# Performance work log

Measured on AMD Instinct MI355X. Metric: run time of the kernel, lower is better.

Reference implementation:

```python
import jax, jax.numpy as jnp
import numpy as np
import math

V, D, H, L, F, S, B = 32000, 1024, 16, 6, 4096, 1024, 2
HD = D // H
EPS = 1e-5


def _pos_encoding(seq_len, d_model):
    pos = np.arange(seq_len, dtype=np.float32)[:, None]
    div = np.exp(np.arange(0, d_model, 2, dtype=np.float32) * (-math.log(10000.0) / d_model))
    pe = np.zeros((seq_len, d_model), dtype=np.float32)
    pe[:, 0::2] = np.sin(pos * div)
    pe[:, 1::2] = np.cos(pos * div)
    return jnp.asarray(pe)


def setup_inputs() -> dict:
    key = jax.random.key(0)
    ks = jax.random.split(key, 24)
    s = 0.02
    emb = jax.random.normal(ks[0], (V, D), jnp.float32) * s
    emb = emb.at[0].set(0.0)  # padding_idx=0
    return {
        "input_ids": jax.random.randint(ks[1], (B, S), 0, V),
        "emb": emb,
        "Wq": jax.random.normal(ks[2], (L, D, D), jnp.float32) * s,
        "bq": jnp.zeros((L, D), jnp.float32),
        "Wk": jax.random.normal(ks[3], (L, D, D), jnp.float32) * s,
        "bk": jnp.zeros((L, D), jnp.float32),
        "Wv": jax.random.normal(ks[4], (L, D, D), jnp.float32) * s,
        "bv": jnp.zeros((L, D), jnp.float32),
        "Wo": jax.random.normal(ks[5], (L, D, D), jnp.float32) * s,
        "bo": jnp.zeros((L, D), jnp.float32),
        "ln1_g": jnp.ones((L, D), jnp.float32),
        "ln1_b": jnp.zeros((L, D), jnp.float32),
        "ln2_g": jnp.ones((L, D), jnp.float32),
        "ln2_b": jnp.zeros((L, D), jnp.float32),
        "W1": jax.random.normal(ks[6], (L, D, F), jnp.float32) * s,
        "b1": jnp.zeros((L, F), jnp.float32),
        "W2": jax.random.normal(ks[7], (L, F, D), jnp.float32) * s,
        "b2": jnp.zeros((L, D), jnp.float32),
        "fn_g": jnp.ones((D,), jnp.float32),
        "fn_b": jnp.zeros((D,), jnp.float32),
        "Wout": jax.random.normal(ks[8], (D, V), jnp.float32) * s,
        "bout": jnp.zeros((V,), jnp.float32),
    }


def _layernorm(x, g, b):
    m = jnp.mean(x, axis=-1, keepdims=True)
    v = jnp.mean(jnp.square(x - m), axis=-1, keepdims=True)
    return (x - m) * jax.lax.rsqrt(v + EPS) * g + b


def reference(input_ids, emb, Wq, bq, Wk, bk, Wv, bv, Wo, bo,
              ln1_g, ln1_b, ln2_g, ln2_b, W1, b1, W2, b2,
              fn_g, fn_b, Wout, bout):
    b, s = input_ids.shape
    x = emb[input_ids] * math.sqrt(D)          # [B,S,D]
    x = x + _pos_encoding(s, D)[None]           # positional encoding (dropout off: eval)
    causal = jnp.tril(jnp.ones((s, s), dtype=bool))  # True where allowed
    for i in range(L):
        h = _layernorm(x, ln1_g[i], ln1_b[i])
        q = (h @ Wq[i] + bq[i]).reshape(b, s, H, HD).transpose(0, 2, 1, 3)
        k = (h @ Wk[i] + bk[i]).reshape(b, s, H, HD).transpose(0, 2, 1, 3)
        v = (h @ Wv[i] + bv[i]).reshape(b, s, H, HD).transpose(0, 2, 1, 3)
        scores = jnp.einsum('bhqd,bhkd->bhqk', q, k) / math.sqrt(HD)
        scores = jnp.where(causal, scores, -jnp.inf)
        attn = jax.nn.softmax(scores, axis=-1)
        ctx = jnp.einsum('bhqk,bhkd->bhqd', attn, v)
        ctx = ctx.transpose(0, 2, 1, 3).reshape(b, s, D)
        x = x + (ctx @ Wo[i] + bo[i])
        h2 = _layernorm(x, ln2_g[i], ln2_b[i])
        ff = jax.nn.gelu(h2 @ W1[i] + b1[i], approximate=False) @ W2[i] + b2[i]
        x = x + ff
    x = _layernorm(x, fn_g, fn_b)
    logits = x @ Wout + bout                   # [B,S,V]
    return logits
```

## Files before the change

### kernel.cpp

```cpp
#include <hip/hip_runtime.h>
#include <math.h>

#define V_   32000
#define D_   1024
#define H_   16
#define HD_  64
#define L_   6
#define F_   4096
#define S_   1024
#define B_   2
#define MTOK (B_*S_)
#define EPSLN 1e-5f

typedef unsigned short ushort_t;
typedef __attribute__((ext_vector_type(8))) short  s16x8;
typedef __attribute__((ext_vector_type(4))) float  f32x4;
typedef __attribute__((ext_vector_type(4))) unsigned short u16x4;

__device__ __forceinline__ float bf2f(unsigned short u) {
    unsigned int x = ((unsigned int)u) << 16;
    return __builtin_bit_cast(float, x);
}
__device__ __forceinline__ unsigned short f2bf(float f) {
    unsigned int x = __builtin_bit_cast(unsigned int, f);
    unsigned int r = (x + 0x7FFFu + ((x >> 16) & 1u)) >> 16;
    return (unsigned short)r;
}
__device__ __forceinline__ float gelu_f(float x) {
    float y = 0.7978845608f * (x + 0.044715f * x * x * x);
    float t = 1.0f - 2.0f / (__expf(2.0f * y) + 1.0f);
    return 0.5f * x * (1.0f + t);
}

__device__ __forceinline__ float blk_sum(float v, float* sb) {
    #pragma unroll
    for (int o = 32; o; o >>= 1) v += __shfl_xor(v, o, 64);
    int w = threadIdx.x >> 6;
    __syncthreads();
    if ((threadIdx.x & 63) == 0) sb[w] = v;
    __syncthreads();
    return sb[0] + sb[1] + sb[2] + sb[3];
}

template<bool GELU, bool OUTBF>
__global__ __launch_bounds__(512, 2)
void gemm256(const ushort_t* __restrict__ A, int lda,
             const ushort_t* __restrict__ BT, int ldb,
             void* __restrict__ Cv, int ldc,
             const float* __restrict__ bias,
             int M, int N, int K)
{
    int nmt = M >> 8;
    int nwg = gridDim.x * gridDim.y;
    int id  = blockIdx.x + gridDim.x * blockIdx.y;
    int swz = ((nwg & 7) == 0) ? ((id & 7) * (nwg >> 3) + (id >> 3)) : id;
    int m0 = (swz % nmt) << 8;
    int n0 = (swz / nmt) << 8;

    __shared__ __align__(16) ushort_t lA[2][256 * 64];
    __shared__ __align__(16) ushort_t lB[2][256 * 64];

    int tid  = threadIdx.x;
    int lane = tid & 63, wave = tid >> 6;
    int lr = lane & 15, lg = lane >> 4;
    int wm = wave >> 2, wn = wave & 3;

    f32x4 acc[8][4] = {};
    int nkt = K >> 6;

    auto stageu = [&](int buf, int kt, int sel) {
        int k0 = kt << 6;
        const ushort_t* src = (sel < 2) ? A : BT;
        int ld    = (sel < 2) ? lda : ldb;
        int rbase = ((sel < 2) ? m0 : n0) + ((sel & 1) << 7);
        ushort_t* dst = ((sel < 2) ? &lA[buf][0] : &lB[buf][0]) + ((sel & 1) << 13);
        #pragma unroll
        for (int r = 0; r < 2; ++r) {
            int e8  = r * 512 + tid;
            int row = e8 >> 3, slot = e8 & 7;
            int ls  = slot ^ (row & 7);
            const ushort_t* g = src + (size_t)(rbase + row) * ld + k0 + ls * 8;
            __builtin_amdgcn_global_load_lds(
                (const __attribute__((address_space(1))) void*)g,
                (__attribute__((address_space(3))) void*)(dst + e8 * 8), 16, 0, 0);
        }
    };
    auto rdA = [&](int buf, int row, int ks) -> s16x8 {
        int sl = (lg + ks * 4) ^ (row & 7);
        return *(const s16x8*)&lA[buf][row * 64 + sl * 8];
    };
    auto rdB = [&](int buf, int row, int ks) -> s16x8 {
        int sl = (lg + ks * 4) ^ (row & 7);
        return *(const s16x8*)&lB[buf][row * 64 + sl * 8];
    };

    stageu(0, 0, 0); stageu(0, 0, 1); stageu(0, 0, 2); stageu(0, 0, 3);
    if (nkt > 1) {
        stageu(1, 1, 2); stageu(1, 1, 3);
        asm volatile("s_waitcnt vmcnt(4)" ::: "memory");
    } else {
        asm volatile("s_waitcnt vmcnt(0)" ::: "memory");
    }
    __builtin_amdgcn_sched_barrier(0);
    __builtin_amdgcn_s_barrier();

    for (int u = 0; u < nkt; ++u) {
        int cur = u & 1, nxt = cur ^ 1;
        s16x8 af0[4][2], af1[4][2], bf0[2][2], bf1[2][2];

        #pragma unroll
        for (int mf = 0; mf < 4; ++mf)
            #pragma unroll
            for (int ks = 0; ks < 2; ++ks)
                af0[mf][ks] = rdA(cur, wm * 128 + mf * 16 + lr, ks);
        #pragma unroll
        for (int nf = 0; nf < 2; ++nf)
            #pragma unroll
            for (int ks = 0; ks < 2; ++ks) {
                bf0[nf][ks] = rdB(cur, wn * 64 + nf * 16 + lr, ks);
                bf1[nf][ks] = rdB(cur, wn * 64 + 32 + nf * 16 + lr, ks);
            }
        if (u + 1 < nkt) { stageu(nxt, u + 1, 0); stageu(nxt, u + 1, 1); }
        __builtin_amdgcn_s_barrier();
        asm volatile("s_waitcnt lgkmcnt(0)" ::: "memory");
        __builtin_amdgcn_sched_barrier(0);
        __builtin_amdgcn_s_setprio(1);
        #pragma unroll
        for (int mf = 0; mf < 4; ++mf)
            #pragma unroll
            for (int ks = 0; ks < 2; ++ks) {
                #pragma unroll
                for (int nf = 0; nf < 2; ++nf) {
                    acc[mf][nf]     = __builtin_amdgcn_mfma_f32_16x16x32_bf16(
                        af0[mf][ks], bf0[nf][ks], acc[mf][nf], 0, 0, 0);
                    acc[mf][2 + nf] = __builtin_amdgcn_mfma_f32_16x16x32_bf16(
                        af0[mf][ks], bf1[nf][ks], acc[mf][2 + nf], 0, 0, 0);
                }
            }
        __builtin_amdgcn_s_setprio(0);
        __builtin_amdgcn_s_barrier();

        #pragma unroll
        for (int mf = 0; mf < 4; ++mf)
            #pragma unroll
            for (int ks = 0; ks < 2; ++ks)
                af1[mf][ks] = rdA(cur, wm * 128 + 64 + mf * 16 + lr, ks);
        if (u + 2 < nkt) { stageu(cur, u + 2, 2); stageu(cur, u + 2, 3); }
        __builtin_amdgcn_s_barrier();
        asm volatile("s_waitcnt lgkmcnt(0)" ::: "memory");
        __builtin_amdgcn_sched_barrier(0);
        __builtin_amdgcn_s_setprio(1);
        #pragma unroll
        for (int mf = 0; mf < 4; ++mf)
            #pragma unroll
            for (int ks = 0; ks < 2; ++ks) {
                #pragma unroll
                for (int nf = 0; nf < 2; ++nf) {
                    acc[4 + mf][nf]     = __builtin_amdgcn_mfma_f32_16x16x32_bf16(
                        af1[mf][ks], bf0[nf][ks], acc[4 + mf][nf], 0, 0, 0);
                    acc[4 + mf][2 + nf] = __builtin_amdgcn_mfma_f32_16x16x32_bf16(
                        af1[mf][ks], bf1[nf][ks], acc[4 + mf][2 + nf], 0, 0, 0);
                }
            }
        __builtin_amdgcn_s_setprio(0);
        if (u + 2 < nkt) asm volatile("s_waitcnt vmcnt(4)" ::: "memory");
        else             asm volatile("s_waitcnt vmcnt(0)" ::: "memory");
        __builtin_amdgcn_sched_barrier(0);
        __builtin_amdgcn_s_barrier();
    }

    float*    Cf = (float*)Cv;
    ushort_t* Cb = (ushort_t*)Cv;
    #pragma unroll
    for (int mf = 0; mf < 8; ++mf) {
        int gm0 = m0 + wm * 128 + mf * 16 + lg * 4;
        #pragma unroll
        for (int nf = 0; nf < 4; ++nf) {
            int gn = n0 + wn * 64 + nf * 16 + lr;
            float bv = bias ? bias[gn] : 0.f;
            #pragma unroll
            for (int j = 0; j < 4; ++j) {
                float v = acc[mf][nf][j] + bv;
                if (GELU) v = gelu_f(v);
                size_t ci = (size_t)(gm0 + j) * ldc + gn;
                if (OUTBF) Cb[ci] = f2bf(v);
                else       Cf[ci] = v;
            }
        }
    }
}

template<int BN, bool GELU, bool RES, bool OUTBF, bool VOUT>
__global__ __launch_bounds__(256)
void gemm_bt(const ushort_t* __restrict__ A, int lda,
             const ushort_t* __restrict__ BT, int ldb,
             void* __restrict__ Cv, int ldc,
             const float* __restrict__ bias,
             const float* __restrict__ res,
             int M, int N, int K, ushort_t* __restrict__ vtp)
{
    const int BK = 64;
    const int NF = BN / 32;
    int nwg = gridDim.x * gridDim.y;
    int id  = blockIdx.x + gridDim.x * blockIdx.y;
    int swz = ((nwg & 7) == 0) ? ((id & 7) * (nwg >> 3) + (id >> 3)) : id;
    int m0 = (swz % gridDim.x) * 128;
    int n0 = (swz / gridDim.x) * BN;

    __shared__ __align__(16) ushort_t lA[2][128 * BK];
    __shared__ __align__(16) ushort_t lB[2][BN * BK];

    int tid  = threadIdx.x;
    int lane = tid & 63;
    int wave = tid >> 6;
    int lr = lane & 15, lg = lane >> 4;
    int wr = wave >> 1, wc = wave & 1;

    f32x4 acc[4][NF] = {};
    int nkt = K / BK;

    auto stage = [&](int buf, int kt) {
        int k0 = kt * BK;
        #pragma unroll
        for (int i = 0; i < 4; ++i) {
            int e8  = i * 256 + tid;
            int row = e8 >> 3, slot = e8 & 7;
            int ls  = slot ^ (row & 7);
            const ushort_t* g = A + (size_t)(m0 + row) * lda + k0 + ls * 8;
            __builtin_amdgcn_global_load_lds(
                (const __attribute__((address_space(1))) void*)g,
                (__attribute__((address_space(3))) void*)&lA[buf][e8 * 8], 16, 0, 0);
        }
        #pragma unroll
        for (int i = 0; i < BN / 32; ++i) {
            int e8  = i * 256 + tid;
            int row = e8 >> 3, slot = e8 & 7;
            int ls  = slot ^ (row & 7);
            const ushort_t* g = BT + (size_t)(n0 + row) * ldb + k0 + ls * 8;
            __builtin_amdgcn_global_load_lds(
                (const __attribute__((address_space(1))) void*)g,
                (__attribute__((address_space(3))) void*)&lB[buf][e8 * 8], 16, 0, 0);
        }
    };

    stage(0, 0);
    __syncthreads();

    int cur = 0;
    for (int kt = 0; kt < nkt; ++kt) {
        if (kt + 1 < nkt) stage(cur ^ 1, kt + 1);
        __builtin_amdgcn_sched_barrier(0);
        s16x8 af[4][2], bfr[NF][2];
        #pragma unroll
        for (int m = 0; m < 4; ++m) {
            int row = wr * 64 + m * 16 + lr;
            #pragma unroll
            for (int ks = 0; ks < 2; ++ks) {
                int sl = (lg + ks * 4) ^ (row & 7);
                af[m][ks] = *(const s16x8*)&lA[cur][row * BK + sl * 8];
            }
        }
        #pragma unroll
        for (int n = 0; n < NF; ++n) {
            int row = wc * (BN / 2) + n * 16 + lr;
            #pragma unroll
            for (int ks = 0; ks < 2; ++ks) {
                int sl = (lg + ks * 4) ^ (row & 7);
                bfr[n][ks] = *(const s16x8*)&lB[cur][row * BK + sl * 8];
            }
        }
        __builtin_amdgcn_s_setprio(1);
        #pragma unroll
        for (int m = 0; m < 4; ++m)
            #pragma unroll
            for (int n = 0; n < NF; ++n)
                #pragma unroll
                for (int ks = 0; ks < 2; ++ks)
                    acc[m][n] = __builtin_amdgcn_mfma_f32_16x16x32_bf16(
                        af[m][ks], bfr[n][ks], acc[m][n], 0, 0, 0);
        __builtin_amdgcn_s_setprio(0);
        __syncthreads();
        cur ^= 1;
    }

    float*    Cf = (float*)Cv;
    ushort_t* Cb = (ushort_t*)Cv;
    #pragma unroll
    for (int m = 0; m < 4; ++m) {
        int gm0 = m0 + wr * 64 + m * 16 + lg * 4;
        #pragma unroll
        for (int n = 0; n < NF; ++n) {
            int gn = n0 + wc * (BN / 2) + n * 16 + lr;
            #pragma unroll
            for (int j = 0; j < 4; ++j) {
                float v = acc[m][n][j];
                if (bias) v += bias[gn];
                size_t ci = (size_t)(gm0 + j) * ldc + gn;
                if (RES)  v += res[ci];
                if (GELU) v = gelu_f(v);
                if (OUTBF) Cb[ci] = f2bf(v);
                else       Cf[ci] = v;
                if (VOUT && gn >= 2048) {
                    int hv = gn - 2048;
                    int mm = gm0 + j;
                    vtp[((size_t)(((mm >> 10) << 4) + (hv >> 6)) * 64
                         + (hv & 63)) * 1024 + (mm & 1023)] = f2bf(v);
                }
            }
        }
    }
}

__global__ __launch_bounds__(256)
void flash_attn(const ushort_t* __restrict__ qkv,
                const ushort_t* __restrict__ vt,
                ushort_t* __restrict__ ctx)
{
    const int QB = 64, KB = 64;
    int z  = blockIdx.y;
    int b  = z >> 4, hh = z & 15;

    __shared__ __align__(16) ushort_t Qs[QB * 64];
    __shared__ __align__(16) ushort_t Ks[2][KB * 64];
    __shared__ __align__(16) ushort_t Vs[2][64 * KB];
    __shared__ float    Ss[QB][68];
    __shared__ __align__(16) ushort_t Ps[QB][72];
    __shared__ float mrow[QB], lrow[QB], arow[QB];

    int tid  = threadIdx.x;
    int lane = tid & 63, wave = tid >> 6;
    int lr = lane & 15, lg = lane >> 4;
    int r = tid >> 2, p = tid & 3;

    auto stageKV = [&](int buf, int kv0) {
        const ushort_t* kbase = qkv + (size_t)(b * S_ + kv0) * 3072 + 1024 + hh * HD_;
        const ushort_t* vbase = vt + (size_t)z * HD_ * S_ + kv0;
        #pragma unroll
        for (int rnd = 0; rnd < 2; ++rnd) {
            int e8 = rnd * 256 + tid;
            int row = e8 >> 3, slot = e8 & 7;
            int ls = slot ^ (row & 7);
            const ushort_t* gk = kbase + (size_t)row * 3072 + ls * 8;
            __builtin_amdgcn_global_load_lds(
                (const __attribute__((address_space(1))) void*)gk,
                (__attribute__((address_space(3))) void*)&Ks[buf][e8 * 8], 16, 0, 0);
            const ushort_t* gv = vbase + (size_t)row * S_ + ls * 8;
            __builtin_amdgcn_global_load_lds(
                (const __attribute__((address_space(1))) void*)gv,
                (__attribute__((address_space(3))) void*)&Vs[buf][e8 * 8], 16, 0, 0);
        }
    };

    #pragma unroll
    for (int half = 0; half < 2; ++half) {
        int qt = half ? (15 - (int)blockIdx.x) : (int)blockIdx.x;
        int q0 = qt * QB;

        if (tid < QB) { mrow[tid] = -1e30f; lrow[tid] = 0.f; }
        const ushort_t* qbase = qkv + (size_t)(b * S_ + q0) * 3072 + hh * HD_;
        #pragma unroll
        for (int rnd = 0; rnd < 2; ++rnd) {
            int e8   = rnd * 256 + tid;
            int row  = e8 >> 3;
            int slot = e8 & 7;
            int ls   = slot ^ (row & 7);
            const ushort_t* g = qbase + (size_t)row * 3072 + ls * 8;
            __builtin_amdgcn_global_load_lds(
                (const __attribute__((address_space(1))) void*)g,
                (__attribute__((address_space(3))) void*)&Qs[e8 * 8], 16, 0, 0);
        }
        stageKV(0, 0);
        __syncthreads();

        s16x8 qa[4][2];
        #pragma unroll
        for (int mf = 0; mf < 4; ++mf)
            #pragma unroll
            for (int ks = 0; ks < 2; ++ks) {
                int row = mf * 16 + lr;
                int sl  = (lg + ks * 4) ^ (row & 7);
                qa[mf][ks] = *(const s16x8*)&Qs[row * 64 + sl * 8];
            }

        f32x4 acc[4] = {};
        int kv_end = q0 + QB;
        int cur = 0;
        for (int kv0 = 0; kv0 < kv_end; kv0 += KB) {
            if (kv0 + KB < kv_end) stageKV(cur ^ 1, kv0 + KB);

            s16x8 kb[2];
            #pragma unroll
            for (int ks = 0; ks < 2; ++ks) {
                int row = wave * 16 + lr;
                int sl  = (lg + ks * 4) ^ (row & 7);
                kb[ks] = *(const s16x8*)&Ks[cur][row * 64 + sl * 8];
            }
            f32x4 sa[4] = {};
            __builtin_amdgcn_s_setprio(1);
            #pragma unroll
            for (int mf = 0; mf < 4; ++mf)
                #pragma unroll
                for (int ks = 0; ks < 2; ++ks)
                    sa[mf] = __builtin_amdgcn_mfma_f32_16x16x32_bf16(
                        qa[mf][ks], kb[ks], sa[mf], 0, 0, 0);
            __builtin_amdgcn_s_setprio(0);

            int ki = kv0 + wave * 16 + lr;
            #pragma unroll
            for (int mf = 0; mf < 4; ++mf)
                #pragma unroll
                for (int j = 0; j < 4; ++j) {
                    int qi = q0 + mf * 16 + lg * 4 + j;
                    float s = (ki <= qi) ? sa[mf][j] * 0.125f : -1e30f;
                    Ss[mf * 16 + lg * 4 + j][wave * 16 + lr] = s;
                }
            __syncthreads();

            float mo = mrow[r];
            float sv[16];
            float pm = -1e30f;
            #pragma unroll
            for (int i = 0; i < 16; ++i) {
                sv[i] = Ss[r][p * 16 + i];
                pm = fmaxf(pm, sv[i]);
            }
            pm = fmaxf(pm, __shfl_xor(pm, 1, 64));
            pm = fmaxf(pm, __shfl_xor(pm, 2, 64));
            float M = fmaxf(mo, pm);
            float sum = 0.f;
            s16x8 pk0, pk1;
            #pragma unroll
            for (int i = 0; i < 8; ++i) {
                float e0 = __expf(sv[i] - M);
                float e1 = __expf(sv[i + 8] - M);
                sum += e0 + e1;
                pk0[i] = (short)f2bf(e0);
                pk1[i] = (short)f2bf(e1);
            }
            *(s16x8*)&Ps[r][p * 16]     = pk0;
            *(s16x8*)&Ps[r][p * 16 + 8] = pk1;
            sum += __shfl_xor(sum, 1, 64);
            sum += __shfl_xor(sum, 2, 64);
            if (p == 0) {
                float al = __expf(mo - M);
                arow[r] = al;
                mrow[r] = M;
                lrow[r] = lrow[r] * al + sum;
            }
            __syncthreads();

            #pragma unroll
            for (int mf = 0; mf < 4; ++mf) {
                #pragma unroll
                for (int j = 0; j < 4; ++j)
                    acc[mf][j] *= arow[mf * 16 + lg * 4 + j];
            }
            s16x8 vb[2];
            #pragma unroll
            for (int ks = 0; ks < 2; ++ks) {
                int row = wave * 16 + lr;
                int sl  = (lg + ks * 4) ^ (row & 7);
                vb[ks] = *(const s16x8*)&Vs[cur][row * 64 + sl * 8];
            }
            __builtin_amdgcn_s_setprio(1);
            #pragma unroll
            for (int mf = 0; mf < 4; ++mf)
                #pragma unroll
                for (int ks = 0; ks < 2; ++ks) {
                    s16x8 pa = *(const s16x8*)((const char*)&Ps[0][0]
                                + (mf * 16 + lr) * 144 + lg * 16 + ks * 64);
                    acc[mf] = __builtin_amdgcn_mfma_f32_16x16x32_bf16(
                        pa, vb[ks], acc[mf], 0, 0, 0);
                }
            __builtin_amdgcn_s_setprio(0);
            __syncthreads();
            cur ^= 1;
        }

        #pragma unroll
        for (int mf = 0; mf < 4; ++mf)
            #pragma unroll
            for (int j = 0; j < 4; ++j) {
                int rr = mf * 16 + lg * 4 + j;
                float o = acc[mf][j] / lrow[rr];
                ctx[(size_t)(b * S_ + q0 + rr) * D_ + hh * HD_ + wave * 16 + lr] = f2bf(o);
            }
        __syncthreads();
    }
}

__global__ __launch_bounds__(256)
void prep_layer(const float* __restrict__ Wq, const float* __restrict__ Wk,
                const float* __restrict__ Wv, const float* __restrict__ Wo,
                const float* __restrict__ W1, const float* __restrict__ W2,
                const float* __restrict__ bq, const float* __restrict__ bk,
                const float* __restrict__ bv,
                ushort_t* __restrict__ wqkvT, ushort_t* __restrict__ woT,
                ushort_t* __restrict__ w1T, ushort_t* __restrict__ w2T,
                float* __restrict__ qkvb)
{
    int bid = blockIdx.x;
    if (bid >= 3072) {
        int j = bid - 3072;
        const float* bsrc = (j == 0) ? bq : (j == 1) ? bk : bv;
        int c = threadIdx.x * 4;
        *(f32x4*)&qkvb[j * 1024 + c] = *(const f32x4*)&bsrc[c];
        return;
    }
    __shared__ float t[64][65];
    int tid = threadIdx.x;
    int tx = tid & 63, ty = tid >> 6;
    const float* src; ushort_t* dst; int R, C, c0, r0;
    if (bid < 1024) {
        int mat = bid >> 8, tnum = bid & 255;
        src = (mat == 0) ? Wq : (mat == 1) ? Wk : (mat == 2) ? Wv : Wo;
        dst = (mat < 3) ? (wqkvT + (size_t)mat * D_ * D_) : woT;
        R = D_; C = D_;
        c0 = (tnum & 15) * 64; r0 = (tnum >> 4) * 64;
    } else if (bid < 2048) {
        int tnum = bid - 1024;
        src = W1; dst = w1T; R = D_; C = F_;
        c0 = (tnum & 63) * 64; r0 = (tnum >> 6) * 64;
    } else {
        int tnum = bid - 2048;
        src = W2; dst = w2T; R = F_; C = D_;
        c0 = (tnum & 15) * 64; r0 = (tnum >> 4) * 64;
    }
    #pragma unroll
    for (int i = 0; i < 16; ++i)
        t[ty + i * 4][tx] = src[(size_t)(r0 + ty + i * 4) * C + c0 + tx];
    __syncthreads();
    int u = tid & 31, v = tid >> 5;
    #pragma unroll
    for (int i = 0; i < 8; ++i) {
        int cc = v + i * 8;
        unsigned int val = (unsigned int)f2bf(t[u * 2][cc])
                         | ((unsigned int)f2bf(t[u * 2 + 1][cc]) << 16);
        *(unsigned int*)&dst[(size_t)(c0 + cc) * R + r0 + u * 2] = val;
    }
}

__global__ __launch_bounds__(256)
void tconv(const float* __restrict__ in, ushort_t* __restrict__ out, int R, int C)
{
    __shared__ float t[64][65];
    int c0 = blockIdx.x * 64, r0 = blockIdx.y * 64;
    int tid = threadIdx.x;
    int tx = tid & 63, ty = tid >> 6;
    #pragma unroll
    for (int i = 0; i < 16; ++i)
        t[ty + i * 4][tx] = in[(size_t)(r0 + ty + i * 4) * C + c0 + tx];
    __syncthreads();
    int u = tid & 31, v = tid >> 5;
    #pragma unroll
    for (int i = 0; i < 8; ++i) {
        int cc = v + i * 8;
        unsigned int val = (unsigned int)f2bf(t[u * 2][cc])
                         | ((unsigned int)f2bf(t[u * 2 + 1][cc]) << 16);
        *(unsigned int*)&out[(size_t)(c0 + cc) * R + r0 + u * 2] = val;
    }
}

__global__ __launch_bounds__(256)
void embed_pe(const int* __restrict__ ids, const float* __restrict__ emb,
              float* __restrict__ x)
{
    int row = blockIdx.x;
    int s   = row & (S_ - 1);
    int id  = ids[row];
    int d   = threadIdx.x * 4;
    f32x4 ev = *(const f32x4*)&emb[(size_t)id * D_ + d];
    f32x4 o;
    #pragma unroll
    for (int j = 0; j < 4; ++j) {
        int dd = d + j;
        int i  = dd >> 1;
        float div = expf(-(float)(2 * i) * (9.210340371976184f / 1024.0f));
        float arg = (float)s * div;
        float pe  = (dd & 1) ? cosf(arg) : sinf(arg);
        o[j] = ev[j] * 32.0f + pe;
    }
    *(f32x4*)&x[(size_t)row * D_ + d] = o;
}

__global__ __launch_bounds__(256)
void ln_kernel(const float* __restrict__ x, const float* __restrict__ g,
               const float* __restrict__ b, ushort_t* __restrict__ out)
{
    __shared__ float sb[4];
    int row = blockIdx.x;
    const float* xr = x + (size_t)row * D_;
    int c = threadIdx.x * 4;
    f32x4 v = *(const f32x4*)&xr[c];
    float s = v[0] + v[1] + v[2] + v[3];
    s = blk_sum(s, sb);
    float mean = s * (1.0f / D_);
    f32x4 dv = v - mean;
    float sq = dv[0]*dv[0] + dv[1]*dv[1] + dv[2]*dv[2] + dv[3]*dv[3];
    sq = blk_sum(sq, sb);
    float rstd = rsqrtf(sq * (1.0f / D_) + EPSLN);
    u16x4 o;
    #pragma unroll
    for (int j = 0; j < 4; ++j)
        o[j] = f2bf(dv[j] * rstd * g[c + j] + b[c + j]);
    *(u16x4*)&out[(size_t)row * D_ + c] = o;
}

__global__ void ws_marker(float* o) { o[threadIdx.x] = -777777.0f; }

extern "C" void kernel_launch(void* const* d_in, const int* in_sizes, int n_in,
                              void* d_out, int out_size, void* d_ws, size_t ws_size,
                              hipStream_t stream)
{
    (void)in_sizes; (void)n_in; (void)out_size;
    const int*   ids  = (const int*)d_in[0];
    const float* emb  = (const float*)d_in[1];
    const float* Wq   = (const float*)d_in[2];
    const float* bq   = (const float*)d_in[3];
    const float* Wk   = (const float*)d_in[4];
    const float* bk   = (const float*)d_in[5];
    const float* Wv   = (const float*)d_in[6];
    const float* bv   = (const float*)d_in[7];
    const float* Wo   = (const float*)d_in[8];
    const float* bo   = (const float*)d_in[9];
    const float* ln1g = (const float*)d_in[10];
    const float* ln1b = (const float*)d_in[11];
    const float* ln2g = (const float*)d_in[12];
    const float* ln2b = (const float*)d_in[13];
    const float* W1   = (const float*)d_in[14];
    const float* b1   = (const float*)d_in[15];
    const float* W2   = (const float*)d_in[16];
    const float* b2   = (const float*)d_in[17];
    const float* fng  = (const float*)d_in[18];
    const float* fnb  = (const float*)d_in[19];
    const float* Wout = (const float*)d_in[20];
    const float* bout = (const float*)d_in[21];
    float* out = (float*)d_out;

    char* base = (char*)d_ws;
    size_t off = 0;
    float*    x    = (float*)(base + off);    off += (size_t)MTOK * D_ * 4;
    ushort_t* h    = (ushort_t*)(base + off); off += (size_t)MTOK * D_ * 2;
    ushort_t* qkv  = (ushort_t*)(base + off); off += (size_t)MTOK * 3 * D_ * 2;
    ushort_t* vt   = (ushort_t*)(base + off); off += (size_t)B_ * H_ * HD_ * S_ * 2;
    ushort_t* ctx  = (ushort_t*)(base + off); off += (size_t)MTOK * D_ * 2;
    ushort_t* ff   = (ushort_t*)(base + off); off += (size_t)MTOK * F_ * 2;
    float*    qkvb = (float*)(base + off);    off += 3072 * 4;
    ushort_t* wqkvT= (ushort_t*)(base + off); off += (size_t)3 * D_ * D_ * 2;
    ushort_t* woT  = (ushort_t*)(base + off); off += (size_t)D_ * D_ * 2;
    ushort_t* w1T  = (ushort_t*)(base + off); off += (size_t)D_ * F_ * 2;
    ushort_t* w2T  = (ushort_t*)(base + off); off += (size_t)F_ * D_ * 2;
    ushort_t* wouT = (ushort_t*)(base + off); off += (size_t)V_ * D_ * 2;
    if (ws_size < off) { ws_marker<<<1, 64, 0, stream>>>(out); return; }

    embed_pe<<<MTOK, 256, 0, stream>>>(ids, emb, x);

    for (int i = 0; i < L_; ++i) {
        prep_layer<<<3075, 256, 0, stream>>>(
            Wq + (size_t)i * D_ * D_, Wk + (size_t)i * D_ * D_,
            Wv + (size_t)i * D_ * D_, Wo + (size_t)i * D_ * D_,
            W1 + (size_t)i * D_ * F_, W2 + (size_t)i * F_ * D_,
            bq + i * D_, bk + i * D_, bv + i * D_,
            wqkvT, woT, w1T, w2T, qkvb);

        ln_kernel<<<MTOK, 256, 0, stream>>>(x, ln1g + i * D_, ln1b + i * D_, h);

        gemm_bt<128,false,false,true,true><<<dim3(16, 24), 256, 0, stream>>>(
            h, D_, wqkvT, D_, qkv, 3 * D_, qkvb, nullptr, MTOK, 3 * D_, D_, vt);

        flash_attn<<<dim3(8, B_ * H_), 256, 0, stream>>>(qkv, vt, ctx);

        gemm_bt<64,false,true,false,false><<<dim3(16, 16), 256, 0, stream>>>(
            ctx, D_, woT, D_, x, D_, bo + i * D_, x, MTOK, D_, D_, nullptr);

        ln_kernel<<<MTOK, 256, 0, stream>>>(x, ln2g + i * D_, ln2b + i * D_, h);

        gemm_bt<128,true,false,true,false><<<dim3(16, 32), 256, 0, stream>>>(
            h, D_, w1T, D_, ff, F_, b1 + i * F_, nullptr, MTOK, F_, D_, nullptr);

        gemm_bt<64,false,true,false,false><<<dim3(16, 16), 256, 0, stream>>>(
            ff, F_, w2T, F_, x, D_, b2 + i * D_, x, MTOK, D_, F_, nullptr);
    }

    ln_kernel<<<MTOK, 256, 0, stream>>>(x, fng, fnb, h);
    tconv<<<dim3(500, 16), 256, 0, stream>>>(Wout, wouT, D_, V_);
    gemm256<false,false><<<dim3(8, 125), 512, 0, stream>>>(
        h, D_, wouT, D_, out, V_, bout, MTOK, V_, D_);
}
```

Before: 1.478 ms.

## Batch all layer weight conversions into one upfront launch and retile QKV GEMM

Replaces the per-layer weight transpose/bf16 conversion launches and the separate Wout conversion with a single large prep kernel that converts all six layers plus the output projection into a bigger workspace, falling back to per-layer conversion when the workspace is too small. This cuts many serialized small launches and the tail effects between them, at the cost of more workspace memory. It also switches the QKV GEMM to a 64-wide tile with twice as many blocks to improve CU occupancy.

```diff
diff --git a/kernel.cpp b/kernel.cpp
--- a/kernel.cpp
+++ b/kernel.cpp
@@ -489,42 +489,58 @@
     }
 }
 
+#define DD_ (D_*D_)
+#define DF_ (D_*F_)
+#define WL_ (3*DD_ + DD_ + DF_ + DF_)
 __global__ __launch_bounds__(256)
-void prep_layer(const float* __restrict__ Wq, const float* __restrict__ Wk,
-                const float* __restrict__ Wv, const float* __restrict__ Wo,
-                const float* __restrict__ W1, const float* __restrict__ W2,
-                const float* __restrict__ bq, const float* __restrict__ bk,
-                const float* __restrict__ bv,
-                ushort_t* __restrict__ wqkvT, ushort_t* __restrict__ woT,
-                ushort_t* __restrict__ w1T, ushort_t* __restrict__ w2T,
-                float* __restrict__ qkvb)
+void prep_all(const float* __restrict__ Wq, const float* __restrict__ Wk,
+              const float* __restrict__ Wv, const float* __restrict__ Wo,
+              const float* __restrict__ W1, const float* __restrict__ W2,
+              const float* __restrict__ bq, const float* __restrict__ bk,
+              const float* __restrict__ bv,
+              ushort_t* __restrict__ wAll, float* __restrict__ qkvbAll,
+              int nl,
+              const float* __restrict__ Wout, ushort_t* __restrict__ wouT)
 {
     int bid = blockIdx.x;
-    if (bid >= 3072) {
-        int j = bid - 3072;
-        const float* bsrc = (j == 0) ? bq : (j == 1) ? bk : bv;
-        int c = threadIdx.x * 4;
-        *(f32x4*)&qkvb[j * 1024 + c] = *(const f32x4*)&bsrc[c];
-        return;
-    }
+    int nwl = nl * 3075;
     __shared__ float t[64][65];
     int tid = threadIdx.x;
     int tx = tid & 63, ty = tid >> 6;
     const float* src; ushort_t* dst; int R, C, c0, r0;
-    if (bid < 1024) {
-        int mat = bid >> 8, tnum = bid & 255;
-        src = (mat == 0) ? Wq : (mat == 1) ? Wk : (mat == 2) ? Wv : Wo;
-        dst = (mat < 3) ? (wqkvT + (size_t)mat * D_ * D_) : woT;
-        R = D_; C = D_;
-        c0 = (tnum & 15) * 64; r0 = (tnum >> 4) * 64;
-    } else if (bid < 2048) {
-        int tnum = bid - 1024;
-        src = W1; dst = w1T; R = D_; C = F_;
-        c0 = (tnum & 63) * 64; r0 = (tnum >> 6) * 64;
+
+    if (bid < nwl) {
+        int layer = bid / 3075, sub = bid % 3075;
+        if (sub >= 3072) {
+            int j = sub - 3072;
+            const float* bsrc = ((j == 0) ? bq : (j == 1) ? bk : bv) + (size_t)layer * D_;
+            int c = tid * 4;
+            *(f32x4*)&qkvbAll[(size_t)layer * 3072 + j * 1024 + c] = *(const f32x4*)&bsrc[c];
+            return;
+        }
+        ushort_t* wl = wAll + (size_t)layer * WL_;
+        if (sub < 1024) {
+            int mat = sub >> 8, tnum = sub & 255;
+            src = ((mat == 0) ? Wq : (mat == 1) ? Wk : (mat == 2) ? Wv : Wo)
+                  + (size_t)layer * DD_;
+            dst = (mat < 3) ? (wl + (size_t)mat * DD_) : (wl + 3 * (size_t)DD_);
+            R = D_; C = D_;
+            c0 = (tnum & 15) * 64; r0 = (tnum >> 4) * 64;
+        } else if (sub < 2048) {
+            int tnum = sub - 1024;
+            src = W1 + (size_t)layer * DF_; dst = wl + 4 * (size_t)DD_;
+            R = D_; C = F_;
+            c0 = (tnum & 63) * 64; r0 = (tnum >> 6) * 64;
+        } else {
+            int tnum = sub - 2048;
+            src = W2 + (size_t)layer * DF_; dst = wl + 4 * (size_t)DD_ + (size_t)DF_;
+            R = F_; C = D_;
+            c0 = (tnum & 15) * 64; r0 = (tnum >> 4) * 64;
+        }
     } else {
-        int tnum = bid - 2048;
-        src = W2; dst = w2T; R = F_; C = D_;
-        c0 = (tnum & 15) * 64; r0 = (tnum >> 4) * 64;
+        int tnum = bid - nwl;
+        src = Wout; dst = wouT; R = D_; C = V_;
+        c0 = (tnum % 500) * 64; r0 = (tnum / 500) * 64;
     }
     #pragma unroll
     for (int i = 0; i < 16; ++i)
@@ -645,27 +661,40 @@
     ushort_t* vt   = (ushort_t*)(base + off); off += (size_t)B_ * H_ * HD_ * S_ * 2;
     ushort_t* ctx  = (ushort_t*)(base + off); off += (size_t)MTOK * D_ * 2;
     ushort_t* ff   = (ushort_t*)(base + off); off += (size_t)MTOK * F_ * 2;
-    float*    qkvb = (float*)(base + off);    off += 3072 * 4;
-    ushort_t* wqkvT= (ushort_t*)(base + off); off += (size_t)3 * D_ * D_ * 2;
-    ushort_t* woT  = (ushort_t*)(base + off); off += (size_t)D_ * D_ * 2;
-    ushort_t* w1T  = (ushort_t*)(base + off); off += (size_t)D_ * F_ * 2;
-    ushort_t* w2T  = (ushort_t*)(base + off); off += (size_t)F_ * D_ * 2;
+    float*    qkvbA= (float*)(base + off);    off += (size_t)L_ * 3072 * 4;
     ushort_t* wouT = (ushort_t*)(base + off); off += (size_t)V_ * D_ * 2;
-    if (ws_size < off) { ws_marker<<<1, 64, 0, stream>>>(out); return; }
+    ushort_t* wAll = (ushort_t*)(base + off);
+    size_t off_small = off + (size_t)WL_ * 2;
+    size_t off_big   = off + (size_t)L_ * WL_ * 2;
+    bool big = (ws_size >= off_big);
+    if (!big && ws_size < off_small) { ws_marker<<<1, 64, 0, stream>>>(out); return; }
 
     embed_pe<<<MTOK, 256, 0, stream>>>(ids, emb, x);
 
+    if (big) {
+        prep_all<<<L_ * 3075 + 8000, 256, 0, stream>>>(
+            Wq, Wk, Wv, Wo, W1, W2, bq, bk, bv, wAll, qkvbA, L_, Wout, wouT);
+    }
+
     for (int i = 0; i < L_; ++i) {
-        prep_layer<<<3075, 256, 0, stream>>>(
-            Wq + (size_t)i * D_ * D_, Wk + (size_t)i * D_ * D_,
-            Wv + (size_t)i * D_ * D_, Wo + (size_t)i * D_ * D_,
-            W1 + (size_t)i * D_ * F_, W2 + (size_t)i * F_ * D_,
-            bq + i * D_, bk + i * D_, bv + i * D_,
-            wqkvT, woT, w1T, w2T, qkvb);
+        ushort_t* wl    = wAll + (big ? (size_t)i * WL_ : 0);
+        float*    qkvb  = qkvbA + (big ? (size_t)i * 3072 : 0);
+        if (!big) {
+            prep_all<<<3075, 256, 0, stream>>>(
+                Wq + (size_t)i * DD_, Wk + (size_t)i * DD_,
+                Wv + (size_t)i * DD_, Wo + (size_t)i * DD_,
+                W1 + (size_t)i * DF_, W2 + (size_t)i * DF_,
+                bq + i * D_, bk + i * D_, bv + i * D_,
+                wl, qkvb, 1, nullptr, nullptr);
+        }
+        ushort_t* wqkvT = wl;
+        ushort_t* woT   = wl + 3 * (size_t)DD_;
+        ushort_t* w1T   = wl + 4 * (size_t)DD_;
+        ushort_t* w2T   = wl + 4 * (size_t)DD_ + (size_t)DF_;
 
         ln_kernel<<<MTOK, 256, 0, stream>>>(x, ln1g + i * D_, ln1b + i * D_, h);
 
-        gemm_bt<128,false,false,true,true><<<dim3(16, 24), 256, 0, stream>>>(
+        gemm_bt<64,false,false,true,true><<<dim3(16, 48), 256, 0, stream>>>(
             h, D_, wqkvT, D_, qkv, 3 * D_, qkvb, nullptr, MTOK, 3 * D_, D_, vt);
 
         flash_attn<<<dim3(8, B_ * H_), 256, 0, stream>>>(qkv, vt, ctx);
@@ -683,7 +712,7 @@
     }
 
     ln_kernel<<<MTOK, 256, 0, stream>>>(x, fng, fnb, h);
-    tconv<<<dim3(500, 16), 256, 0, stream>>>(Wout, wouT, D_, V_);
+    if (!big) tconv<<<dim3(500, 16), 256, 0, stream>>>(Wout, wouT, D_, V_);
     gemm256<false,false><<<dim3(8, 125), 512, 0, stream>>>(
         h, D_, wouT, D_, out, V_, bout, MTOK, V_, D_);
 }
```

After: 1.596 ms. 8.0% more time.
